# Optimization experiments

Measured on AMD Instinct MI355X. Metric: run time of the kernel, lower is better.

Reference implementation:

```python
import jax, jax.numpy as jnp
import numpy as np

N_NODES = 1024
NUM_MOL = 32
ATOMS = 32          # atoms per molecule
SDIM = 256
VDIM = 64
EDIM = 128
NUM_BOND_TYPES = 5


def _fully_connected_edges():
    # all ordered pairs (j, i), j != i, within each molecule block
    idx = np.arange(ATOMS)
    jj, ii = np.meshgrid(idx, idx, indexing='ij')
    mask = jj != ii
    jj, ii = jj[mask], ii[mask]                      # [ATOMS*(ATOMS-1)]
    offs = (np.arange(NUM_MOL) * ATOMS)[:, None]
    j_all = (jj[None, :] + offs).reshape(-1)
    i_all = (ii[None, :] + offs).reshape(-1)
    return np.stack([j_all, i_all]).astype(np.int32)  # [2, E]


def setup_inputs() -> dict:
    key = jax.random.key(0)
    ks = jax.random.split(key, 12)
    edge_index = jnp.asarray(_fully_connected_edges())  # [2, 31744]
    E = edge_index.shape[1]
    inp = {
        's': jax.random.normal(ks[0], (N_NODES, SDIM), jnp.float32),
        'v': jax.random.normal(ks[1], (N_NODES, 3, VDIM), jnp.float32),
        'p': jax.random.normal(ks[2], (N_NODES, 3), jnp.float32),
        'e': jax.random.normal(ks[3], (E, EDIM), jnp.float32),
        'batch': jnp.repeat(jnp.arange(NUM_MOL, dtype=jnp.int32), ATOMS),
        'edge_index': edge_index,
        # learned parameters
        'W_shared': jax.random.normal(ks[4], (SDIM, SDIM), jnp.float32) * 0.02,
        'b_shared': jnp.zeros((SDIM,), jnp.float32),
        'W_coords': jax.random.normal(ks[5], (VDIM, 1), jnp.float32) * 0.02,
        'W_bond': jax.random.normal(ks[6], (EDIM, SDIM), jnp.float32) * 0.02,
        'b_bond': jnp.zeros((SDIM,), jnp.float32),
        'W_b0': jax.random.normal(ks[7], (SDIM + 1, SDIM), jnp.float32) * 0.02,
        'b_b0': jnp.zeros((SDIM,), jnp.float32),
        'W_b1': jax.random.normal(ks[8], (SDIM, NUM_BOND_TYPES), jnp.float32) * 0.02,
        'b_b1': jnp.zeros((NUM_BOND_TYPES,), jnp.float32),
    }
    return inp


def reference(s, v, p, e, batch, edge_index,
              W_shared, b_shared, W_coords, W_bond, b_bond,
              W_b0, b_b0, W_b1, b_b1):
    n = s.shape[0]
    # shared_mapping: DenseLayer with SiLU
    s = jax.nn.silu(s @ W_shared + b_shared)
    # coords_lin: [n,3,vdim] @ [vdim,1] -> [n,3]
    coords = p + jnp.einsum('ncv,vo->nc', v, W_coords)
    # scatter_mean centering per molecule
    seg_sum = jax.ops.segment_sum(coords, batch, num_segments=NUM_MOL)
    counts = jax.ops.segment_sum(jnp.ones((n, 1), coords.dtype), batch,
                                 num_segments=NUM_MOL)
    mean = seg_sum / jnp.maximum(counts, 1.0)
    coords = coords - mean[batch]
    # dense symmetrization of edge features
    j, i = edge_index[0], edge_index[1]
    e_dense = jnp.zeros((n, n, e.shape[-1]), e.dtype).at[j, i].set(e)
    e_dense = 0.5 * (e_dense + jnp.swapaxes(e_dense, 0, 1))
    e_sym = e_dense[j, i]                                  # [E, EDIM]
    # squared distance per edge
    d = jnp.sum((coords[i] - coords[j]) ** 2, axis=-1, keepdims=True)  # [E,1]
    # edge MLP
    f = s[i] + s[j] + (e_sym @ W_bond + b_bond)            # [E, SDIM]
    edge = jnp.concatenate([f, d], axis=-1)                # [E, SDIM+1]
    h = jax.nn.silu(edge @ W_b0 + b_b0)
    bonds_pred = h @ W_b1 + b_b1                           # [E, 5]
    return bonds_pred
```

## Files before the change

### kernel.cpp

```cpp
#include <hip/hip_runtime.h>
#include <hip/hip_bf16.h>

#define N_NODES 1024
#define NUM_MOL 32
#define ATOMS 32
#define SDIM 256
#define VDIM 64
#define EDIM 128
#define NBT 5
#define EDGES_PER_MOL (ATOMS * (ATOMS - 1))
#define PAIRS_PER_MOL (ATOMS * (ATOMS - 1) / 2)
#define N_PAIRS (NUM_MOL * PAIRS_PER_MOL)

typedef __attribute__((ext_vector_type(8))) short bf16x8;
typedef __attribute__((ext_vector_type(4))) float f32x4;

__device__ __forceinline__ unsigned short f2bf(float x) {
    union { float f; unsigned int u; } v; v.f = x;
    unsigned int r = v.u + 0x7fffu + ((v.u >> 16) & 1u);
    return (unsigned short)(r >> 16);
}

__device__ __forceinline__ bf16x8 pack8(const float4& x0, const float4& x1) {
    bf16x8 r;
    r[0] = (short)f2bf(x0.x); r[1] = (short)f2bf(x0.y);
    r[2] = (short)f2bf(x0.z); r[3] = (short)f2bf(x0.w);
    r[4] = (short)f2bf(x1.x); r[5] = (short)f2bf(x1.y);
    r[6] = (short)f2bf(x1.z); r[7] = (short)f2bf(x1.w);
    return r;
}

__global__ __launch_bounds__(256) void prep_kernel(
    const float* __restrict__ s, const float* __restrict__ Ws,
    const float* __restrict__ Wb0,
    const float* __restrict__ Wbond, const float* __restrict__ bbond,
    const float* __restrict__ bb0,
    const float* __restrict__ v, const float* __restrict__ p,
    const float* __restrict__ Wc,
    unsigned short* __restrict__ Wsf, unsigned short* __restrict__ Wb0f,
    unsigned short* __restrict__ sbf, unsigned short* __restrict__ Wf,
    float* __restrict__ bcomb, float* __restrict__ coords)
{
    __shared__ __align__(16) float smem[1024 + 16];
    const int t   = threadIdx.x;
    const int bid = blockIdx.x;

    if (bid < 64) {
        const float* W = (bid < 32) ? Ws : Wb0;
        unsigned short* dst = (bid < 32) ? Wsf : Wb0f;
        const int g    = ((bid & 31) << 8) + t;
        const int lane = g & 63;
        const int kt   = (g >> 6) & 7;
        const int nt   = g >> 9;
        const int n     = nt * 16 + (lane & 15);
        const int kbase = kt * 32 + (lane >> 4) * 8;
        const float* col = W + (size_t)kbase * SDIM + n;
        bf16x8 r;
#pragma unroll
        for (int e2 = 0; e2 < 8; ++e2) r[e2] = (short)f2bf(col[(size_t)e2 * SDIM]);
        *(bf16x8*)&dst[(size_t)g * 8] = r;

    } else if (bid < 192) {
        const int g    = ((bid - 64) << 8) + t;
        const int lane = g & 63;
        const int kt   = (g >> 6) & 7;
        const int rb   = g >> 9;
        const int row   = rb * 16 + (lane & 15);
        const int kbase = kt * 32 + (lane >> 4) * 8;
        const float* srow = s + (size_t)row * SDIM + kbase;
        const float4 x0 = *(const float4*)(srow);
        const float4 x1 = *(const float4*)(srow + 4);
        *(bf16x8*)&sbf[(size_t)g * 8] = pack8(x0, x1);

    } else if (bid < 224) {
        float (*wb)[SDIM] = (float (*)[SDIM])smem;
        const int r0 = (bid - 192) * 4;
        for (int r = 0; r < 4; ++r) wb[r][t] = Wbond[(r0 + r) * SDIM + t];
        __syncthreads();

        float acc[4];
#pragma unroll
        for (int r = 0; r < 4; ++r) acc[r] = 0.f;
        for (int c = 0; c < SDIM; c += 4) {
            const float w0 = Wb0[(c + 0) * SDIM + t];
            const float w1 = Wb0[(c + 1) * SDIM + t];
            const float w2 = Wb0[(c + 2) * SDIM + t];
            const float w3 = Wb0[(c + 3) * SDIM + t];
#pragma unroll
            for (int r = 0; r < 4; ++r) {
                const float4 wv = *(const float4*)&wb[r][c];
                acc[r] += wv.x * w0 + wv.y * w1 + wv.z * w2 + wv.w * w3;
            }
        }
        const int nt = t >> 4;
#pragma unroll
        for (int r = 0; r < 4; ++r) {
            const int k = r0 + r;
            const int kt = k >> 5, g = (k >> 3) & 3, eidx = k & 7;
            const int lane = (t & 15) + 16 * g;
            Wf[((size_t)((nt * 4 + kt) * 64 + lane)) * 8 + eidx] = f2bf(0.5f * acc[r]);
        }

    } else if (bid < 256) {
        const int mol = bid - 224;
        float* cl   = smem;
        float* mean = smem + 100;
        if (t < ATOMS * 3) {
            const int a = t / 3, dim = t % 3;
            const int node = mol * ATOMS + a;
            const float* vv = v + (size_t)node * 3 * VDIM + dim * VDIM;
            float acc = 0.f;
#pragma unroll 8
            for (int k = 0; k < VDIM; ++k) acc += vv[k] * Wc[k];
            cl[a * 3 + dim] = p[node * 3 + dim] + acc;
        }
        __syncthreads();
        if (t < 3) {
            float sum = 0.f;
            for (int a = 0; a < ATOMS; ++a) sum += cl[a * 3 + t];
            mean[t] = sum * (1.f / ATOMS);
        }
        __syncthreads();
        if (t < ATOMS * 3) {
            const int a = t / 3, dim = t % 3;
            coords[(mol * ATOMS + a) * 3 + dim] = cl[a * 3 + dim] - mean[dim];
        }
    } else {
        float acc = bb0[t];
#pragma unroll 8
        for (int m = 0; m < SDIM; ++m) acc += bbond[m] * Wb0[m * SDIM + t];
        bcomb[t] = acc;
    }
}

__global__ __launch_bounds__(256) void node_kernel(
    const unsigned short* __restrict__ sbf,
    const unsigned short* __restrict__ Wsf,
    const unsigned short* __restrict__ Wb0f,
    const float* __restrict__ bs,
    float* __restrict__ sp2)
{
    __shared__ __align__(16) unsigned short s2u[16 * 256];
    const int t = threadIdx.x;
    const int w = t >> 6, l = t & 63;
    const int kg = l >> 4, lr = l & 15;
    const int bid = blockIdx.x;
    const int r0 = bid * 16;

    const bf16x8* sfp = (const bf16x8*)sbf;
    bf16x8 a[8];
#pragma unroll
    for (int kt = 0; kt < 8; ++kt) a[kt] = sfp[(bid * 8 + kt) * 64 + l];

    const bf16x8* wsp = (const bf16x8*)Wsf;
    f32x4 acc[4];
#pragma unroll
    for (int q = 0; q < 4; ++q) {
        acc[q][0] = 0.f; acc[q][1] = 0.f; acc[q][2] = 0.f; acc[q][3] = 0.f;
        const int nt = w * 4 + q;
#pragma unroll
        for (int kt = 0; kt < 8; ++kt) {
            const bf16x8 bf = wsp[(nt * 8 + kt) * 64 + l];
            acc[q] = __builtin_amdgcn_mfma_f32_16x16x32_bf16(a[kt], bf, acc[q], 0, 0, 0);
        }
    }

#pragma unroll
    for (int q = 0; q < 4; ++q) {
        const int n = (w * 4 + q) * 16 + lr;
        const float bsv = bs[n];
#pragma unroll
        for (int j = 0; j < 4; ++j) {
            const int row = kg * 4 + j;
            const float x = acc[q][j] + bsv;
            const float sl = x / (1.f + __expf(-x));
            s2u[(row * 256 + n) ^ ((row & 7) << 3)] = f2bf(sl);
        }
    }
    __syncthreads();

#pragma unroll
    for (int kt = 0; kt < 8; ++kt) {
        const int idx = (lr * 256 + kt * 32 + kg * 8) ^ ((lr & 7) << 3);
        a[kt] = *(const bf16x8*)&s2u[idx];
    }

    const bf16x8* wbp = (const bf16x8*)Wb0f;
#pragma unroll
    for (int q = 0; q < 4; ++q) {
        acc[q][0] = 0.f; acc[q][1] = 0.f; acc[q][2] = 0.f; acc[q][3] = 0.f;
        const int nt = w * 4 + q;
#pragma unroll
        for (int kt = 0; kt < 8; ++kt) {
            const bf16x8 bf = wbp[(nt * 8 + kt) * 64 + l];
            acc[q] = __builtin_amdgcn_mfma_f32_16x16x32_bf16(a[kt], bf, acc[q], 0, 0, 0);
        }
    }
#pragma unroll
    for (int q = 0; q < 4; ++q) {
        const int n = (w * 4 + q) * 16 + lr;
#pragma unroll
        for (int j = 0; j < 4; ++j)
            sp2[(size_t)(r0 + kg * 4 + j) * SDIM + n] = acc[q][j];
    }
}

#define PB 16
__global__ __launch_bounds__(256) void edge_mfma_kernel(
    const float* __restrict__ sp2, const float* __restrict__ coords,
    const float* __restrict__ e, const unsigned short* __restrict__ Wf,
    const float* __restrict__ bcomb, const float* __restrict__ Wb0,
    const float* __restrict__ Wb1, const float* __restrict__ bb1,
    float* __restrict__ out)
{
    __shared__ __align__(16) float spsum[PB][260];
    __shared__ __align__(16) unsigned short esym[PB * EDIM];
    __shared__ float wb1s[SDIM * NBT];
    __shared__ float bb1s[8];
    __shared__ int   ksh[PB], krevsh[PB], ish[PB], jsh[PB];
    __shared__ float dsh[PB];

    const int t = threadIdx.x;
    const int bid = (blockIdx.x & 7) * 124 + (blockIdx.x >> 3);
    const int P0  = bid * PB;

    for (int idx = t; idx < SDIM * NBT; idx += 256) wb1s[idx] = Wb1[idx];
    if (t < NBT) bb1s[t] = bb1[t];
    if (t < PB) {
        const int P   = P0 + t;
        const int mol = P / PAIRS_PER_MOL;
        const int p   = P - mol * PAIRS_PER_MOL;
        int jj = (int)((63.0f - sqrtf((float)(3969 - 8 * p))) * 0.5f);
        if (jj < 0) jj = 0;
        if (jj > 30) jj = 30;
        while (jj > 0 && (63 * jj - jj * jj) / 2 > p) --jj;
        while (jj < 30 && (63 * (jj + 1) - (jj + 1) * (jj + 1)) / 2 <= p) ++jj;
        const int Ojj = (63 * jj - jj * jj) / 2;
        const int ii  = jj + 1 + (p - Ojj);
        const int q    = jj * 31 + (ii - 1);
        const int qrev = ii * 31 + jj;
        ksh[t]    = mol * EDGES_PER_MOL + q;
        krevsh[t] = mol * EDGES_PER_MOL + qrev;
        const int i = mol * ATOMS + ii, j = mol * ATOMS + jj;
        ish[t] = i; jsh[t] = j;
        const float dx = coords[i * 3 + 0] - coords[j * 3 + 0];
        const float dy = coords[i * 3 + 1] - coords[j * 3 + 1];
        const float dz = coords[i * 3 + 2] - coords[j * 3 + 2];
        dsh[t] = dx * dx + dy * dy + dz * dz;
    }
    __syncthreads();

    {
        const int r  = t >> 4;
        const int c8 = (t & 15) * 8;
        const float* ek  = e + (size_t)ksh[r] * EDIM + c8;
        const float* ekr = e + (size_t)krevsh[r] * EDIM + c8;
        const float4 x0 = *(const float4*)(ek);
        const float4 x1 = *(const float4*)(ek + 4);
        const float4 y0 = *(const float4*)(ekr);
        const float4 y1 = *(const float4*)(ekr + 4);

        const int c0 = (t & 15) * 4;
        const float* ai = sp2 + (size_t)ish[r] * SDIM;
        const float* aj = sp2 + (size_t)jsh[r] * SDIM;
        const float* w2 = Wb0 + (size_t)SDIM * SDIM;
        const float d = dsh[r];
#pragma unroll
        for (int i = 0; i < 4; ++i) {
            const int c = c0 + 64 * i;
            const float4 a4 = *(const float4*)(ai + c);
            const float4 b4 = *(const float4*)(aj + c);
            const float4 w4 = *(const float4*)(w2 + c);
            const float4 g4 = *(const float4*)(bcomb + c);
            float4 rv;
            rv.x = a4.x + b4.x + d * w4.x + g4.x;
            rv.y = a4.y + b4.y + d * w4.y + g4.y;
            rv.z = a4.z + b4.z + d * w4.z + g4.z;
            rv.w = a4.w + b4.w + d * w4.w + g4.w;
            *(float4*)&spsum[r][c] = rv;
        }

        float4 sx, sy;
        sx.x = x0.x + y0.x; sx.y = x0.y + y0.y; sx.z = x0.z + y0.z; sx.w = x0.w + y0.w;
        sy.x = x1.x + y1.x; sy.y = x1.y + y1.y; sy.z = x1.z + y1.z; sy.w = x1.w + y1.w;
        const int idx = (r * EDIM + c8) ^ ((r & 7) << 3);
        *(bf16x8*)&esym[idx] = pack8(sx, sy);
    }
    __syncthreads();

    const int w = t >> 6, l = t & 63;
    const int kg = l >> 4, lr = l & 15;

    bf16x8 afrag[4];
#pragma unroll
    for (int kt = 0; kt < 4; ++kt) {
        const int idx = (lr * EDIM + kt * 32 + kg * 8) ^ ((lr & 7) << 3);
        afrag[kt] = *(const bf16x8*)&esym[idx];
    }

    const bf16x8* wfp = (const bf16x8*)Wf;
    f32x4 acc[4];
#pragma unroll
    for (int q = 0; q < 4; ++q) {
        acc[q][0] = 0.f; acc[q][1] = 0.f; acc[q][2] = 0.f; acc[q][3] = 0.f;
        const int nt = w * 4 + q;
        const bf16x8 b0 = wfp[(nt * 4 + 0) * 64 + l];
        const bf16x8 b1 = wfp[(nt * 4 + 1) * 64 + l];
        const bf16x8 b2 = wfp[(nt * 4 + 2) * 64 + l];
        const bf16x8 b3 = wfp[(nt * 4 + 3) * 64 + l];
        acc[q] = __builtin_amdgcn_mfma_f32_16x16x32_bf16(afrag[0], b0, acc[q], 0, 0, 0);
        acc[q] = __builtin_amdgcn_mfma_f32_16x16x32_bf16(afrag[1], b1, acc[q], 0, 0, 0);
        acc[q] = __builtin_amdgcn_mfma_f32_16x16x32_bf16(afrag[2], b2, acc[q], 0, 0, 0);
        acc[q] = __builtin_amdgcn_mfma_f32_16x16x32_bf16(afrag[3], b3, acc[q], 0, 0, 0);
    }

#pragma unroll
    for (int q = 0; q < 4; ++q) {
        const int n = (w * 4 + q) * 16 + lr;
#pragma unroll
        for (int j = 0; j < 4; ++j) {
            const int r = kg * 4 + j;
            const float x = acc[q][j] + spsum[r][n];
            spsum[r][n] = x / (1.f + __expf(-x));
        }
    }
    __syncthreads();

    if (t < PB * NBT * 2) {
        const int task = t >> 1, half = t & 1;
        const int r  = task / NBT;
        const int tt = task - r * NBT;
        float a = half ? 0.f : bb1s[tt];
        const int base = half * 32;
#pragma unroll 4
        for (int cc = 0; cc < 32; ++cc) {
            const int c4 = base + ((cc + task) & 31);
            const int c  = c4 * 4;
            const float4 hv = *(const float4*)&spsum[r][c];
            a += hv.x * wb1s[(c + 0) * NBT + tt] + hv.y * wb1s[(c + 1) * NBT + tt] +
                 hv.z * wb1s[(c + 2) * NBT + tt] + hv.w * wb1s[(c + 3) * NBT + tt];
        }
        a += __shfl_xor(a, 1);
        if (!half) {
            out[(size_t)ksh[r] * NBT + tt]    = a;
            out[(size_t)krevsh[r] * NBT + tt] = a;
        }
    }
}

extern "C" void kernel_launch(void* const* d_in, const int* in_sizes, int n_in,
                              void* d_out, int out_size, void* d_ws, size_t ws_size,
                              hipStream_t stream)
{
    const float* s        = (const float*)d_in[0];
    const float* v        = (const float*)d_in[1];
    const float* p        = (const float*)d_in[2];
    const float* e        = (const float*)d_in[3];
    const float* W_shared = (const float*)d_in[6];
    const float* b_shared = (const float*)d_in[7];
    const float* W_coords = (const float*)d_in[8];
    const float* W_bond   = (const float*)d_in[9];
    const float* b_bond   = (const float*)d_in[10];
    const float* W_b0     = (const float*)d_in[11];
    const float* b_b0     = (const float*)d_in[12];
    const float* W_b1     = (const float*)d_in[13];
    const float* b_b1     = (const float*)d_in[14];
    float* out = (float*)d_out;

    char* ws = (char*)d_ws;
    float*          sp2    = (float*)(ws + 0);
    unsigned short* Wsf    = (unsigned short*)(ws + 1048576);
    unsigned short* Wb0f   = (unsigned short*)(ws + 1179648);
    unsigned short* sbf    = (unsigned short*)(ws + 1310720);
    unsigned short* Wf     = (unsigned short*)(ws + 1835008);
    float*          bcomb  = (float*)(ws + 1900544);
    float*          coords = (float*)(ws + 1901568);

    prep_kernel<<<257, 256, 0, stream>>>(s, W_shared, W_b0, W_bond, b_bond, b_b0,
                                         v, p, W_coords,
                                         Wsf, Wb0f, sbf, Wf, bcomb, coords);
    node_kernel<<<64, 256, 0, stream>>>(sbf, Wsf, Wb0f, b_shared, sp2);
    edge_mfma_kernel<<<N_PAIRS / PB, 256, 0, stream>>>(sp2, coords, e, Wf, bcomb,
                                                       W_b0, W_b1, b_b1, out);
}
```

Measured before the change: 34.02 us.

## Restructure prep stages: slim weight-pack kernel, fuse s-conversion and Wbond·Wb0 into node kernel

The prep kernel now only packs W_shared and W_b0 into the bf16 MFMA layout. The node kernel converts s to bf16 directly in registers, which drops the intermediate sbf buffer. The fp32 scalar Wbond@Wb0 product becomes an MFMA GEMM using the packed Wb0f, and the coords and bias blocks run alongside in the same launch. This shortens the critical path of the first kernel and cuts a global round trip, but the Wbond@Wb0 product now uses bf16 inputs instead of fp32, which adds some precision error.

```diff
diff --git a/kernel.cpp b/kernel.cpp
--- a/kernel.cpp
+++ b/kernel.cpp
@@ -31,80 +31,150 @@
 }
 
 __global__ __launch_bounds__(256) void prep_kernel(
-    const float* __restrict__ s, const float* __restrict__ Ws,
-    const float* __restrict__ Wb0,
+    const float* __restrict__ Ws, const float* __restrict__ Wb0,
+    unsigned short* __restrict__ Wsf, unsigned short* __restrict__ Wb0f)
+{
+    const int t   = threadIdx.x;
+    const int bid = blockIdx.x;
+    const float* W = (bid < 32) ? Ws : Wb0;
+    unsigned short* dst = (bid < 32) ? Wsf : Wb0f;
+    const int g    = ((bid & 31) << 8) + t;
+    const int lane = g & 63;
+    const int kt   = (g >> 6) & 7;
+    const int nt   = g >> 9;
+    const int n     = nt * 16 + (lane & 15);
+    const int kbase = kt * 32 + (lane >> 4) * 8;
+    const float* col = W + (size_t)kbase * SDIM + n;
+    bf16x8 r;
+#pragma unroll
+    for (int e2 = 0; e2 < 8; ++e2) r[e2] = (short)f2bf(col[(size_t)e2 * SDIM]);
+    *(bf16x8*)&dst[(size_t)g * 8] = r;
+}
+
+__global__ __launch_bounds__(256) void node_kernel(
+    const float* __restrict__ s,
+    const unsigned short* __restrict__ Wsf,
+    const unsigned short* __restrict__ Wb0f,
+    const float* __restrict__ bs,
     const float* __restrict__ Wbond, const float* __restrict__ bbond,
-    const float* __restrict__ bb0,
+    const float* __restrict__ Wb0, const float* __restrict__ bb0,
     const float* __restrict__ v, const float* __restrict__ p,
     const float* __restrict__ Wc,
-    unsigned short* __restrict__ Wsf, unsigned short* __restrict__ Wb0f,
-    unsigned short* __restrict__ sbf, unsigned short* __restrict__ Wf,
-    float* __restrict__ bcomb, float* __restrict__ coords)
+    float* __restrict__ sp2, unsigned short* __restrict__ Wf,
+    float* __restrict__ coords, float* __restrict__ bcomb)
 {
-    __shared__ __align__(16) float smem[1024 + 16];
-    const int t   = threadIdx.x;
+    __shared__ __align__(16) unsigned short s2u[16 * 256];
+    const int t = threadIdx.x;
     const int bid = blockIdx.x;
+    const int w = t >> 6, l = t & 63;
+    const int kg = l >> 4, lr = l & 15;
 
     if (bid < 64) {
-        const float* W = (bid < 32) ? Ws : Wb0;
-        unsigned short* dst = (bid < 32) ? Wsf : Wb0f;
-        const int g    = ((bid & 31) << 8) + t;
-        const int lane = g & 63;
-        const int kt   = (g >> 6) & 7;
-        const int nt   = g >> 9;
-        const int n     = nt * 16 + (lane & 15);
-        const int kbase = kt * 32 + (lane >> 4) * 8;
-        const float* col = W + (size_t)kbase * SDIM + n;
-        bf16x8 r;
-#pragma unroll
-        for (int e2 = 0; e2 < 8; ++e2) r[e2] = (short)f2bf(col[(size_t)e2 * SDIM]);
-        *(bf16x8*)&dst[(size_t)g * 8] = r;
-
-    } else if (bid < 192) {
-        const int g    = ((bid - 64) << 8) + t;
-        const int lane = g & 63;
-        const int kt   = (g >> 6) & 7;
-        const int rb   = g >> 9;
-        const int row   = rb * 16 + (lane & 15);
-        const int kbase = kt * 32 + (lane >> 4) * 8;
-        const float* srow = s + (size_t)row * SDIM + kbase;
-        const float4 x0 = *(const float4*)(srow);
-        const float4 x1 = *(const float4*)(srow + 4);
-        *(bf16x8*)&sbf[(size_t)g * 8] = pack8(x0, x1);
-
-    } else if (bid < 224) {
-        float (*wb)[SDIM] = (float (*)[SDIM])smem;
-        const int r0 = (bid - 192) * 4;
-        for (int r = 0; r < 4; ++r) wb[r][t] = Wbond[(r0 + r) * SDIM + t];
+        const int r0 = bid * 16;
+
+        bf16x8 a[8];
+        const float* srow = s + (size_t)(r0 + lr) * SDIM + kg * 8;
+#pragma unroll
+        for (int kt = 0; kt < 8; ++kt) {
+            const float4 x0 = *(const float4*)(srow + kt * 32);
+            const float4 x1 = *(const float4*)(srow + kt * 32 + 4);
+            a[kt] = pack8(x0, x1);
+        }
+
+        const bf16x8* wsp = (const bf16x8*)Wsf;
+        f32x4 acc[4];
+#pragma unroll
+        for (int q = 0; q < 4; ++q) {
+            acc[q][0] = 0.f; acc[q][1] = 0.f; acc[q][2] = 0.f; acc[q][3] = 0.f;
+            const int nt = w * 4 + q;
+#pragma unroll
+            for (int kt = 0; kt < 8; ++kt) {
+                const bf16x8 bf = wsp[(nt * 8 + kt) * 64 + l];
+                acc[q] = __builtin_amdgcn_mfma_f32_16x16x32_bf16(a[kt], bf, acc[q], 0, 0, 0);
+            }
+        }
+
+#pragma unroll
+        for (int q = 0; q < 4; ++q) {
+            const int n = (w * 4 + q) * 16 + lr;
+            const float bsv = bs[n];
+#pragma unroll
+            for (int j = 0; j < 4; ++j) {
+                const int row = kg * 4 + j;
+                const float x = acc[q][j] + bsv;
+                const float sl = x / (1.f + __expf(-x));
+                s2u[(row * 256 + n) ^ ((row & 7) << 3)] = f2bf(sl);
+            }
+        }
         __syncthreads();
 
-        float acc[4];
-#pragma unroll
-        for (int r = 0; r < 4; ++r) acc[r] = 0.f;
-        for (int c = 0; c < SDIM; c += 4) {
-            const float w0 = Wb0[(c + 0) * SDIM + t];
-            const float w1 = Wb0[(c + 1) * SDIM + t];
-            const float w2 = Wb0[(c + 2) * SDIM + t];
-            const float w3 = Wb0[(c + 3) * SDIM + t];
-#pragma unroll
-            for (int r = 0; r < 4; ++r) {
-                const float4 wv = *(const float4*)&wb[r][c];
-                acc[r] += wv.x * w0 + wv.y * w1 + wv.z * w2 + wv.w * w3;
-            }
-        }
-        const int nt = t >> 4;
-#pragma unroll
-        for (int r = 0; r < 4; ++r) {
-            const int k = r0 + r;
-            const int kt = k >> 5, g = (k >> 3) & 3, eidx = k & 7;
-            const int lane = (t & 15) + 16 * g;
-            Wf[((size_t)((nt * 4 + kt) * 64 + lane)) * 8 + eidx] = f2bf(0.5f * acc[r]);
-        }
-
-    } else if (bid < 256) {
-        const int mol = bid - 224;
-        float* cl   = smem;
-        float* mean = smem + 100;
+#pragma unroll
+        for (int kt = 0; kt < 8; ++kt) {
+            const int idx = (lr * 256 + kt * 32 + kg * 8) ^ ((lr & 7) << 3);
+            a[kt] = *(const bf16x8*)&s2u[idx];
+        }
+
+        const bf16x8* wbp = (const bf16x8*)Wb0f;
+#pragma unroll
+        for (int q = 0; q < 4; ++q) {
+            acc[q][0] = 0.f; acc[q][1] = 0.f; acc[q][2] = 0.f; acc[q][3] = 0.f;
+            const int nt = w * 4 + q;
+#pragma unroll
+            for (int kt = 0; kt < 8; ++kt) {
+                const bf16x8 bf = wbp[(nt * 8 + kt) * 64 + l];
+                acc[q] = __builtin_amdgcn_mfma_f32_16x16x32_bf16(a[kt], bf, acc[q], 0, 0, 0);
+            }
+        }
+#pragma unroll
+        for (int q = 0; q < 4; ++q) {
+            const int n = (w * 4 + q) * 16 + lr;
+#pragma unroll
+            for (int j = 0; j < 4; ++j)
+                sp2[(size_t)(r0 + kg * 4 + j) * SDIM + n] = acc[q][j];
+        }
+
+    } else if (bid < 72) {
+        const int r0 = (bid - 64) * 16;
+
+        bf16x8 a[8];
+        const float* wrow = Wbond + (size_t)(r0 + lr) * SDIM + kg * 8;
+#pragma unroll
+        for (int kt = 0; kt < 8; ++kt) {
+            const float4 x0 = *(const float4*)(wrow + kt * 32);
+            const float4 x1 = *(const float4*)(wrow + kt * 32 + 4);
+            a[kt] = pack8(x0, x1);
+        }
+
+        const bf16x8* wbp = (const bf16x8*)Wb0f;
+        f32x4 acc[4];
+#pragma unroll
+        for (int q = 0; q < 4; ++q) {
+            acc[q][0] = 0.f; acc[q][1] = 0.f; acc[q][2] = 0.f; acc[q][3] = 0.f;
+            const int nt = w * 4 + q;
+#pragma unroll
+            for (int kt = 0; kt < 8; ++kt) {
+                const bf16x8 bf = wbp[(nt * 8 + kt) * 64 + l];
+                acc[q] = __builtin_amdgcn_mfma_f32_16x16x32_bf16(a[kt], bf, acc[q], 0, 0, 0);
+            }
+        }
+
+#pragma unroll
+        for (int q = 0; q < 4; ++q) {
+            const int nt2 = w * 4 + q;
+#pragma unroll
+            for (int j = 0; j < 4; ++j) {
+                const int krow = r0 + kg * 4 + j;
+                const int kt2 = krow >> 5, g2 = (krow >> 3) & 3, eidx = krow & 7;
+                const int lane2 = lr + 16 * g2;
+                Wf[((size_t)((nt2 * 4 + kt2) * 64 + lane2)) * 8 + eidx] =
+                    f2bf(0.5f * acc[q][j]);
+            }
+        }
+
+    } else if (bid < 104) {
+        const int mol = bid - 72;
+        float* cl   = (float*)s2u;
+        float* mean = (float*)s2u + 100;
         if (t < ATOMS * 3) {
             const int a = t / 3, dim = t % 3;
             const int node = mol * ATOMS + a;
@@ -127,81 +197,9 @@
         }
     } else {
         float acc = bb0[t];
-#pragma unroll 8
+#pragma unroll 16
         for (int m = 0; m < SDIM; ++m) acc += bbond[m] * Wb0[m * SDIM + t];
         bcomb[t] = acc;
-    }
-}
-
-__global__ __launch_bounds__(256) void node_kernel(
-    const unsigned short* __restrict__ sbf,
-    const unsigned short* __restrict__ Wsf,
-    const unsigned short* __restrict__ Wb0f,
-    const float* __restrict__ bs,
-    float* __restrict__ sp2)
-{
-    __shared__ __align__(16) unsigned short s2u[16 * 256];
-    const int t = threadIdx.x;
-    const int w = t >> 6, l = t & 63;
-    const int kg = l >> 4, lr = l & 15;
-    const int bid = blockIdx.x;
-    const int r0 = bid * 16;
-
-    const bf16x8* sfp = (const bf16x8*)sbf;
-    bf16x8 a[8];
-#pragma unroll
-    for (int kt = 0; kt < 8; ++kt) a[kt] = sfp[(bid * 8 + kt) * 64 + l];
-
-    const bf16x8* wsp = (const bf16x8*)Wsf;
-    f32x4 acc[4];
-#pragma unroll
-    for (int q = 0; q < 4; ++q) {
-        acc[q][0] = 0.f; acc[q][1] = 0.f; acc[q][2] = 0.f; acc[q][3] = 0.f;
-        const int nt = w * 4 + q;
-#pragma unroll
-        for (int kt = 0; kt < 8; ++kt) {
-            const bf16x8 bf = wsp[(nt * 8 + kt) * 64 + l];
-            acc[q] = __builtin_amdgcn_mfma_f32_16x16x32_bf16(a[kt], bf, acc[q], 0, 0, 0);
-        }
-    }
-
-#pragma unroll
-    for (int q = 0; q < 4; ++q) {
-        const int n = (w * 4 + q) * 16 + lr;
-        const float bsv = bs[n];
-#pragma unroll
-        for (int j = 0; j < 4; ++j) {
-            const int row = kg * 4 + j;
-            const float x = acc[q][j] + bsv;
-            const float sl = x / (1.f + __expf(-x));
-            s2u[(row * 256 + n) ^ ((row & 7) << 3)] = f2bf(sl);
-        }
-    }
-    __syncthreads();
-
-#pragma unroll
-    for (int kt = 0; kt < 8; ++kt) {
-        const int idx = (lr * 256 + kt * 32 + kg * 8) ^ ((lr & 7) << 3);
-        a[kt] = *(const bf16x8*)&s2u[idx];
-    }
-
-    const bf16x8* wbp = (const bf16x8*)Wb0f;
-#pragma unroll
-    for (int q = 0; q < 4; ++q) {
-        acc[q][0] = 0.f; acc[q][1] = 0.f; acc[q][2] = 0.f; acc[q][3] = 0.f;
-        const int nt = w * 4 + q;
-#pragma unroll
-        for (int kt = 0; kt < 8; ++kt) {
-            const bf16x8 bf = wbp[(nt * 8 + kt) * 64 + l];
-            acc[q] = __builtin_amdgcn_mfma_f32_16x16x32_bf16(a[kt], bf, acc[q], 0, 0, 0);
-        }
-    }
-#pragma unroll
-    for (int q = 0; q < 4; ++q) {
-        const int n = (w * 4 + q) * 16 + lr;
-#pragma unroll
-        for (int j = 0; j < 4; ++j)
-            sp2[(size_t)(r0 + kg * 4 + j) * SDIM + n] = acc[q][j];
     }
 }
 
@@ -371,15 +369,15 @@
     float*          sp2    = (float*)(ws + 0);
     unsigned short* Wsf    = (unsigned short*)(ws + 1048576);
     unsigned short* Wb0f   = (unsigned short*)(ws + 1179648);
-    unsigned short* sbf    = (unsigned short*)(ws + 1310720);
-    unsigned short* Wf     = (unsigned short*)(ws + 1835008);
-    float*          bcomb  = (float*)(ws + 1900544);
-    float*          coords = (float*)(ws + 1901568);
-
-    prep_kernel<<<257, 256, 0, stream>>>(s, W_shared, W_b0, W_bond, b_bond, b_b0,
+    unsigned short* Wf     = (unsigned short*)(ws + 1310720);
+    float*          bcomb  = (float*)(ws + 1376256);
+    float*          coords = (float*)(ws + 1377280);
+
+    prep_kernel<<<64, 256, 0, stream>>>(W_shared, W_b0, Wsf, Wb0f);
+    node_kernel<<<105, 256, 0, stream>>>(s, Wsf, Wb0f, b_shared,
+                                         W_bond, b_bond, W_b0, b_b0,
                                          v, p, W_coords,
-                                         Wsf, Wb0f, sbf, Wf, bcomb, coords);
-    node_kernel<<<64, 256, 0, stream>>>(sbf, Wsf, Wb0f, b_shared, sp2);
+                                         sp2, Wf, coords, bcomb);
     edge_mfma_kernel<<<N_PAIRS / PB, 256, 0, stream>>>(sp2, coords, e, Wf, bcomb,
                                                        W_b0, W_b1, b_b1, out);
 }
```

New measurement: 28.12 us (median of 2 runs). -17.4%, faster.
